# Kernel tuning notes

Measured on AMD Instinct MI355X. Metric: run time of the kernel, lower is better.

## Reference

```python
import jax, jax.numpy as jnp
import numpy as np

LOG_2PI = float(np.log(2.0 * np.pi))


def setup_inputs() -> dict:
    key = jax.random.key(0)
    k1, k2, k3 = jax.random.split(key, 3)
    N, M, D = 8192, 4096, 784
    samples = jax.random.normal(k1, (N, D), dtype=jnp.float32)
    x = jax.random.normal(k2, (M, D), dtype=jnp.float32)
    # per-feature std, kept away from zero for numerical sanity
    std = jax.random.uniform(k3, (D,), dtype=jnp.float32, minval=0.5, maxval=1.5)
    return {"samples": samples, "x": x, "std": std}


def reference(samples, x, std):
    # Diagonal-Gaussian mixture log-prob:
    #   logp[n, m] = sum_d [ -0.5*((s_nd - x_md)/std_d)^2 - 0.5*log(2*pi) - log(std_d) ]
    # computed via the ||u||^2 + ||v||^2 - 2 u.v identity on std-scaled vectors
    # (mathematically identical to the torch broadcast, without the (N,M,D) tensor).
    N, D = samples.shape
    M = x.shape[0]
    u = samples / std  # (N, D)
    v = x / std        # (M, D)
    sq_dist = (
        jnp.sum(u * u, axis=1)[:, None]
        + jnp.sum(v * v, axis=1)[None, :]
        - 2.0 * jnp.einsum("nd,md->nm", u, v)
    )  # (N, M)
    log_const = -0.5 * D * LOG_2PI - jnp.sum(jnp.log(std))
    log_prob = -0.5 * sq_dist + log_const  # (N, M)
    # logsumexp over mixture components, minus log(M)
    return jax.nn.logsumexp(log_prob, axis=1) - jnp.log(jnp.asarray(M, dtype=samples.dtype))
```

## Files before the change

### kernel.cpp

```cpp
#include <hip/hip_runtime.h>
#include <cstdint>
#include <cstddef>


#define N_ROWS 8192
#define M_ROWS 4096
#define D_DIM  784
#define KPB    896
#define LOG2PI 1.8378770664093453f
#define LOGM   8.317766166719343f

typedef unsigned char u8;
typedef __attribute__((ext_vector_type(8))) int   i32x8;
typedef __attribute__((ext_vector_type(4))) float f32x4;

__device__ __forceinline__ void gld16(const u8* g, u8* l) {
    __builtin_amdgcn_global_load_lds(
        (__attribute__((address_space(1))) void*)(void*)g,
        (__attribute__((address_space(3))) void*)l, 16, 0, 0);
}

__global__ __launch_bounds__(256) void k_prep(const float* __restrict__ samples,
                                              const float* __restrict__ x,
                                              const float* __restrict__ stdv,
                                              u8* __restrict__ dst,
                                              float* __restrict__ norm) {
    const int wid = threadIdx.x >> 6, lane = threadIdx.x & 63;
    const int row0 = blockIdx.x * 8 + wid * 2;

    float4 rstd[4];
#pragma unroll
    for (int i = 0; i < 4; ++i) {
        int c = lane + 64 * i;
        rstd[i] = make_float4(1.f, 1.f, 1.f, 1.f);
        if (c < 196) {
            float4 d = ((const float4*)stdv)[c];
            rstd[i] = make_float4(1.f / d.x, 1.f / d.y, 1.f / d.z, 1.f / d.w);
        }
    }

#pragma unroll
    for (int rr = 0; rr < 2; ++rr) {
        const int row = row0 + rr;
        const float* src = (row < N_ROWS) ? samples + (size_t)row * D_DIM
                                          : x + (size_t)(row - N_ROWS) * D_DIM;
        unsigned* drow = (unsigned*)(dst + (size_t)row * KPB);
        float sq = 0.f;
#pragma unroll
        for (int i = 0; i < 4; ++i) {
            const int c = lane + 64 * i;
            if (c < 224) {
                unsigned p = 0;
                if (c < 196) {
                    float4 s = ((const float4*)src)[c];
                    float ux = s.x * rstd[i].x, uy = s.y * rstd[i].y;
                    float uz = s.z * rstd[i].z, uw = s.w * rstd[i].w;
                    p = __builtin_amdgcn_cvt_pk_fp8_f32(ux, uy, 0, false);
                    p = __builtin_amdgcn_cvt_pk_fp8_f32(uz, uw, p, true);
                    float r0 = __builtin_amdgcn_cvt_f32_fp8(p, 0);
                    float r1 = __builtin_amdgcn_cvt_f32_fp8(p, 1);
                    float r2 = __builtin_amdgcn_cvt_f32_fp8(p, 2);
                    float r3 = __builtin_amdgcn_cvt_f32_fp8(p, 3);
                    sq += r0 * r0 + r1 * r1 + r2 * r2 + r3 * r3;
                }
                drow[c] = p;
            }
        }
        for (int m = 32; m; m >>= 1) sq += __shfl_xor(sq, m);
        if (lane == 0) norm[row] = sq;
    }
}

__global__ __launch_bounds__(512, 2) void k_gemm(const u8* __restrict__ U,
                                                 const u8* __restrict__ V,
                                                 const float* __restrict__ vnorm,
                                                 float* __restrict__ pmax,
                                                 float* __restrict__ psum) {
    __shared__ __align__(16) char smem[131072];
    float2* part = (float2*)smem;

    const int tid = threadIdx.x;
    const int lane = tid & 63;
    const int wid = tid >> 6;
    const int waveRow = wid >> 2;
    const int waveCol = wid & 3;
    const int bCol = blockIdx.x;
    const int bRow = blockIdx.y;
    const int g = lane >> 4, rl = lane & 15;

    const int r16 = lane >> 2, sl = lane & 3;
    const int gc16 = sl ^ ((r16 >> 1) & 3);
    const u8* gA[2]; const u8* gB[2]; int lo[2];
#pragma unroll
    for (int q = 0; q < 2; ++q) {
        const int rg = wid * 2 + q;
        gA[q] = U + (size_t)(bRow * 256 + rg * 16 + r16) * KPB + gc16 * 16;
        gB[q] = V + (size_t)(bCol * 256 + rg * 16 + r16) * KPB + gc16 * 16;
        lo[q] = rg * 1024;
    }

    const int key = (rl >> 1) & 3;
    const int slotLo = (2 * (g & 1)) ^ key;
    const int aoff = (g >> 1) * 32768 + (waveRow * 128 + rl) * 64 + slotLo * 16;
    const int boff = (g >> 1) * 32768 + 16384 + (waveCol * 64 + rl) * 64 + slotLo * 16;

    f32x4 acc[8][4];
#pragma unroll
    for (int i = 0; i < 8; ++i)
#pragma unroll
        for (int j = 0; j < 4; ++j) acc[i][j] = (f32x4){0.f, 0.f, 0.f, 0.f};

#define ISSUE(u) { \
    u8* lb = (u8*)smem + ((u) & 3) * 32768; \
    const int ko = (u) * 64; \
    gld16(gA[0] + ko, lb + lo[0]); \
    gld16(gB[0] + ko, lb + 16384 + lo[0]); \
    gld16(gA[1] + ko, lb + lo[1]); \
    gld16(gB[1] + ko, lb + 16384 + lo[1]); }

    ISSUE(0); ISSUE(1); ISSUE(2);

#pragma unroll
    for (int T = 0; T < 7; ++T) {
        if (T < 6) ISSUE(2 * T + 3);
        if (T < 6) __builtin_amdgcn_s_waitcnt(0x0F78);
        else       __builtin_amdgcn_s_waitcnt(0x0F70);
        __builtin_amdgcn_s_barrier();

        const char* base = smem + (T & 1) * 65536;
        i32x8 b[4], a[2];
#pragma unroll
        for (int ph = 0; ph < 4; ++ph) {
            if (ph == 0) {
#pragma unroll
                for (int j = 0; j < 4; ++j) {
                    int4 L = *(const int4*)(base + (boff + j * 1024));
                    int4 H = *(const int4*)(base + ((boff + j * 1024) ^ 16));
                    b[j] = (i32x8){L.x, L.y, L.z, L.w, H.x, H.y, H.z, H.w};
                }
            }
#pragma unroll
            for (int t = 0; t < 2; ++t) {
                const int i = ph * 2 + t;
                int4 L = *(const int4*)(base + (aoff + i * 1024));
                int4 H = *(const int4*)(base + ((aoff + i * 1024) ^ 16));
                a[t] = (i32x8){L.x, L.y, L.z, L.w, H.x, H.y, H.z, H.w};
            }
            __builtin_amdgcn_s_barrier();
            __builtin_amdgcn_s_waitcnt(0xC07F);
            __builtin_amdgcn_s_setprio(1);
#pragma unroll
            for (int t = 0; t < 2; ++t)
#pragma unroll
                for (int j = 0; j < 4; ++j)
                    acc[ph * 2 + t][j] = __builtin_amdgcn_mfma_scale_f32_16x16x128_f8f6f4(
                        a[t], b[j], acc[ph * 2 + t][j], 0 , 0 ,
                        0, 127 , 0, 127 );
            __builtin_amdgcn_s_setprio(0);
            __builtin_amdgcn_s_barrier();
        }
        if (T < 5) ISSUE(2 * T + 4);
    }
#undef ISSUE
    __syncthreads();

    float vn[4];
#pragma unroll
    for (int j = 0; j < 4; ++j) vn[j] = vnorm[bCol * 256 + waveCol * 64 + j * 16 + rl];

    const int prow0 = waveRow * 128 + g * 4;
    const int pc = waveCol * 16 + rl;
#pragma unroll
    for (int i = 0; i < 8; ++i) {
#pragma unroll
        for (int rg = 0; rg < 4; ++rg) {
            float w0 = acc[i][0][rg] - 0.5f * vn[0];
            float w1 = acc[i][1][rg] - 0.5f * vn[1];
            float w2 = acc[i][2][rg] - 0.5f * vn[2];
            float w3 = acc[i][3][rg] - 0.5f * vn[3];
            float m = fmaxf(fmaxf(w0, w1), fmaxf(w2, w3));
            float s = __expf(w0 - m) + __expf(w1 - m) + __expf(w2 - m) + __expf(w3 - m);
            part[(prow0 + i * 16 + rg) * 64 + pc] = make_float2(m, s);
        }
    }
    __syncthreads();
    if (tid < 256) {
        const float2* p = part + tid * 64;
        const int rot = tid & 63;
        float m = -3.4e38f;
#pragma unroll 8
        for (int q = 0; q < 64; ++q) m = fmaxf(m, p[(q + rot) & 63].x);
        float s = 0.f;
#pragma unroll 8
        for (int q = 0; q < 64; ++q) { float2 v = p[(q + rot) & 63]; s += v.y * __expf(v.x - m); }
        size_t grow = (size_t)(bRow * 256 + tid);
        pmax[grow * 16 + bCol] = m;
        psum[grow * 16 + bCol] = s;
    }
}

__global__ __launch_bounds__(256) void k_final(const float* __restrict__ pmax,
                                               const float* __restrict__ psum,
                                               const float* __restrict__ norm,
                                               const float* __restrict__ stdv,
                                               float* __restrict__ out) {
    __shared__ float wsum[4];
    const int t = threadIdx.x;
    float ls = 0.f;
    for (int d = t; d < D_DIM; d += 256) ls += logf(stdv[d]);
    for (int m = 32; m; m >>= 1) ls += __shfl_xor(ls, m);
    if ((t & 63) == 0) wsum[t >> 6] = ls;
    __syncthreads();
    const float logc = -0.5f * (float)D_DIM * LOG2PI - (wsum[0] + wsum[1] + wsum[2] + wsum[3]);

    const int n = blockIdx.x * 256 + t;
    const float* pm = pmax + (size_t)n * 16;
    const float* ps = psum + (size_t)n * 16;
    float gm = pm[0];
#pragma unroll
    for (int c = 1; c < 16; ++c) gm = fmaxf(gm, pm[c]);
    float S = 0.f;
#pragma unroll
    for (int c = 0; c < 16; ++c) S += ps[c] * __expf(pm[c] - gm);
    out[n] = gm + logf(S) - 0.5f * norm[n] + logc - LOGM;
}

extern "C" void kernel_launch(void* const* d_in, const int* in_sizes, int n_in,
                              void* d_out, int out_size, void* d_ws, size_t ws_size,
                              hipStream_t stream) {
    const float* samples = (const float*)d_in[0];
    const float* x       = (const float*)d_in[1];
    const float* stdv    = (const float*)d_in[2];
    float* out = (float*)d_out;

    char* ws = (char*)d_ws;
    u8*    U    = (u8*)ws;
    u8*    V    = (u8*)(ws + 7340032);
    float* norm = (float*)(ws + 11010048);
    float* pmax = (float*)(ws + 11059200);
    float* psum = (float*)(ws + 11583488);

    k_prep<<<(N_ROWS + M_ROWS) / 8, 256, 0, stream>>>(samples, x, stdv, U, norm);
    k_gemm<<<dim3(M_ROWS / 256, N_ROWS / 256), 512, 0, stream>>>(U, V, norm + N_ROWS, pmax, psum);
    k_final<<<N_ROWS / 256, 256, 0, stream>>>(pmax, psum, norm, stdv, out);
}
```

Measured before the change: 139.2 us.

## Switch GEMM to 32x32x64 FP8 MFMA with 3-stage LDS ring

```diff
diff --git a/kernel.cpp b/kernel.cpp
--- a/kernel.cpp
+++ b/kernel.cpp
@@ -11,8 +11,8 @@
 #define LOGM   8.317766166719343f
 
 typedef unsigned char u8;
-typedef __attribute__((ext_vector_type(8))) int   i32x8;
-typedef __attribute__((ext_vector_type(4))) float f32x4;
+typedef __attribute__((ext_vector_type(8)))  int   i32x8;
+typedef __attribute__((ext_vector_type(16))) float f32x16;
 
 __device__ __forceinline__ void gld16(const u8* g, u8* l) {
     __builtin_amdgcn_global_load_lds(
@@ -86,116 +86,122 @@
     const int waveCol = wid & 3;
     const int bCol = blockIdx.x;
     const int bRow = blockIdx.y;
-    const int g = lane >> 4, rl = lane & 15;
-
-    const int r16 = lane >> 2, sl = lane & 3;
-    const int gc16 = sl ^ ((r16 >> 1) & 3);
+    const int lr = lane & 31, h = lane >> 5;
+
+    const int r4 = lane >> 2;
+    const int gc = (lane & 3) ^ ((lane >> 3) & 3);
     const u8* gA[2]; const u8* gB[2]; int lo[2];
 #pragma unroll
     for (int q = 0; q < 2; ++q) {
-        const int rg = wid * 2 + q;
-        gA[q] = U + (size_t)(bRow * 256 + rg * 16 + r16) * KPB + gc16 * 16;
-        gB[q] = V + (size_t)(bCol * 256 + rg * 16 + r16) * KPB + gc16 * 16;
-        lo[q] = rg * 1024;
-    }
-
-    const int key = (rl >> 1) & 3;
-    const int slotLo = (2 * (g & 1)) ^ key;
-    const int aoff = (g >> 1) * 32768 + (waveRow * 128 + rl) * 64 + slotLo * 16;
-    const int boff = (g >> 1) * 32768 + 16384 + (waveCol * 64 + rl) * 64 + slotLo * 16;
-
-    f32x4 acc[8][4];
-#pragma unroll
-    for (int i = 0; i < 8; ++i)
-#pragma unroll
-        for (int j = 0; j < 4; ++j) acc[i][j] = (f32x4){0.f, 0.f, 0.f, 0.f};
+        const int row = wid * 32 + q * 16 + r4;
+        gA[q] = U + (size_t)(bRow * 256 + row) * KPB + gc * 16;
+        gB[q] = V + (size_t)(bCol * 256 + row) * KPB + gc * 16;
+        lo[q] = wid * 2048 + q * 1024;
+    }
+
+    const int key = (lr >> 1) & 3;
+    const int slotL = (2 * h) ^ key;
+    const int aoff = (waveRow * 128 + lr) * 64 + slotL * 16;
+    const int boff = 16384 + (waveCol * 64 + lr) * 64 + slotL * 16;
+
+    f32x16 acc[4][2];
+#pragma unroll
+    for (int i = 0; i < 4; ++i)
+#pragma unroll
+        for (int j = 0; j < 2; ++j)
+#pragma unroll
+            for (int r = 0; r < 16; ++r) acc[i][j][r] = 0.f;
 
 #define ISSUE(u) { \
-    u8* lb = (u8*)smem + ((u) & 3) * 32768; \
+    u8* lb = (u8*)smem + ((u) % 3) * 32768; \
     const int ko = (u) * 64; \
     gld16(gA[0] + ko, lb + lo[0]); \
     gld16(gB[0] + ko, lb + 16384 + lo[0]); \
     gld16(gA[1] + ko, lb + lo[1]); \
     gld16(gB[1] + ko, lb + 16384 + lo[1]); }
 
-    ISSUE(0); ISSUE(1); ISSUE(2);
-
-#pragma unroll
-    for (int T = 0; T < 7; ++T) {
-        if (T < 6) ISSUE(2 * T + 3);
-        if (T < 6) __builtin_amdgcn_s_waitcnt(0x0F78);
-        else       __builtin_amdgcn_s_waitcnt(0x0F70);
+    ISSUE(0); ISSUE(1);
+
+#pragma unroll
+    for (int kt = 0; kt < 14; ++kt) {
+        if (kt < 12) {
+            ISSUE(kt + 2);
+            __builtin_amdgcn_s_waitcnt(0x0F78);
+        } else if (kt == 12) {
+            __builtin_amdgcn_s_waitcnt(0x0F74);
+        } else {
+            __builtin_amdgcn_s_waitcnt(0x0F70);
+        }
         __builtin_amdgcn_s_barrier();
 
-        const char* base = smem + (T & 1) * 65536;
-        i32x8 b[4], a[2];
-#pragma unroll
-        for (int ph = 0; ph < 4; ++ph) {
-            if (ph == 0) {
-#pragma unroll
-                for (int j = 0; j < 4; ++j) {
-                    int4 L = *(const int4*)(base + (boff + j * 1024));
-                    int4 H = *(const int4*)(base + ((boff + j * 1024) ^ 16));
-                    b[j] = (i32x8){L.x, L.y, L.z, L.w, H.x, H.y, H.z, H.w};
-                }
+        const char* base = smem + (kt % 3) * 32768;
+        i32x8 a[4], b[2];
+#pragma unroll
+        for (int i = 0; i < 4; ++i) {
+            int4 L = *(const int4*)(base + (aoff + i * 2048));
+            int4 H = *(const int4*)(base + ((aoff + i * 2048) ^ 16));
+            a[i] = (i32x8){L.x, L.y, L.z, L.w, H.x, H.y, H.z, H.w};
+        }
+#pragma unroll
+        for (int j = 0; j < 2; ++j) {
+            int4 L = *(const int4*)(base + (boff + j * 2048));
+            int4 H = *(const int4*)(base + ((boff + j * 2048) ^ 16));
+            b[j] = (i32x8){L.x, L.y, L.z, L.w, H.x, H.y, H.z, H.w};
+        }
+#pragma unroll
+        for (int i = 0; i < 4; ++i)
+#pragma unroll
+            for (int j = 0; j < 2; ++j)
+                acc[i][j] = __builtin_amdgcn_mfma_scale_f32_32x32x64_f8f6f4(
+                    a[i], b[j], acc[i][j], 0 , 0 ,
+                    0, 127 , 0, 127 );
+
+        __builtin_amdgcn_s_barrier();
+    }
+#undef ISSUE
+
+    const float vn0 = vnorm[bCol * 256 + waveCol * 64 + lr];
+    const float vn1 = vnorm[bCol * 256 + waveCol * 64 + 32 + lr];
+    __syncthreads();
+
+#pragma unroll
+    for (int i = 0; i < 4; ++i) {
+#pragma unroll
+        for (int r = 0; r < 16; ++r) {
+            float w0 = acc[i][0][r] - 0.5f * vn0;
+            float w1 = acc[i][1][r] - 0.5f * vn1;
+            float m = fmaxf(w0, w1);
+            float s = __expf(w0 - m) + __expf(w1 - m);
+            float mo = __shfl_xor(m, 16);
+            float so = __shfl_xor(s, 16);
+            float M = fmaxf(m, mo);
+            s = s * __expf(m - M) + so * __expf(mo - M);
+            if (lr < 16) {
+                const int rin = (r & 3) + 8 * (r >> 2) + 4 * h;
+                part[(waveRow * 128 + i * 32 + rin) * 64 + (waveCol * 16 + lr)] =
+                    make_float2(M, s);
             }
-#pragma unroll
-            for (int t = 0; t < 2; ++t) {
-                const int i = ph * 2 + t;
-                int4 L = *(const int4*)(base + (aoff + i * 1024));
-                int4 H = *(const int4*)(base + ((aoff + i * 1024) ^ 16));
-                a[t] = (i32x8){L.x, L.y, L.z, L.w, H.x, H.y, H.z, H.w};
-            }
-            __builtin_amdgcn_s_barrier();
-            __builtin_amdgcn_s_waitcnt(0xC07F);
-            __builtin_amdgcn_s_setprio(1);
-#pragma unroll
-            for (int t = 0; t < 2; ++t)
-#pragma unroll
-                for (int j = 0; j < 4; ++j)
-                    acc[ph * 2 + t][j] = __builtin_amdgcn_mfma_scale_f32_16x16x128_f8f6f4(
-                        a[t], b[j], acc[ph * 2 + t][j], 0 , 0 ,
-                        0, 127 , 0, 127 );
-            __builtin_amdgcn_s_setprio(0);
-            __builtin_amdgcn_s_barrier();
-        }
-        if (T < 5) ISSUE(2 * T + 4);
-    }
-#undef ISSUE
+        }
+    }
     __syncthreads();
-
-    float vn[4];
-#pragma unroll
-    for (int j = 0; j < 4; ++j) vn[j] = vnorm[bCol * 256 + waveCol * 64 + j * 16 + rl];
-
-    const int prow0 = waveRow * 128 + g * 4;
-    const int pc = waveCol * 16 + rl;
-#pragma unroll
-    for (int i = 0; i < 8; ++i) {
-#pragma unroll
-        for (int rg = 0; rg < 4; ++rg) {
-            float w0 = acc[i][0][rg] - 0.5f * vn[0];
-            float w1 = acc[i][1][rg] - 0.5f * vn[1];
-            float w2 = acc[i][2][rg] - 0.5f * vn[2];
-            float w3 = acc[i][3][rg] - 0.5f * vn[3];
-            float m = fmaxf(fmaxf(w0, w1), fmaxf(w2, w3));
-            float s = __expf(w0 - m) + __expf(w1 - m) + __expf(w2 - m) + __expf(w3 - m);
-            part[(prow0 + i * 16 + rg) * 64 + pc] = make_float2(m, s);
-        }
-    }
-    __syncthreads();
-    if (tid < 256) {
-        const float2* p = part + tid * 64;
-        const int rot = tid & 63;
+    {
+        const int row = tid >> 1, half = tid & 1;
+        const float2* p = part + row * 64 + half * 32;
         float m = -3.4e38f;
 #pragma unroll 8
-        for (int q = 0; q < 64; ++q) m = fmaxf(m, p[(q + rot) & 63].x);
+        for (int q = 0; q < 32; ++q) m = fmaxf(m, p[(q + row) & 31].x);
         float s = 0.f;
 #pragma unroll 8
-        for (int q = 0; q < 64; ++q) { float2 v = p[(q + rot) & 63]; s += v.y * __expf(v.x - m); }
-        size_t grow = (size_t)(bRow * 256 + tid);
-        pmax[grow * 16 + bCol] = m;
-        psum[grow * 16 + bCol] = s;
+        for (int q = 0; q < 32; ++q) { float2 v = p[(q + row) & 31]; s += v.y * __expf(v.x - m); }
+        float mo = __shfl_xor(m, 1);
+        float so = __shfl_xor(s, 1);
+        float M = fmaxf(m, mo);
+        s = s * __expf(m - M) + so * __expf(mo - M);
+        if (half == 0) {
+            size_t grow = (size_t)(bRow * 256 + row);
+            pmax[grow * 16 + bCol] = M;
+            psum[grow * 16 + bCol] = s;
+        }
     }
 }
 
```

New measurement: 287.7 us. +106.7%, slower.

## Simplify GEMM main loop: whole-tile prefetch, single barrier, interleaved fragment loads

Applied to the files above, without the earlier changes.

```diff
diff --git a/kernel.cpp b/kernel.cpp
--- a/kernel.cpp
+++ b/kernel.cpp
@@ -88,21 +88,22 @@
     const int bRow = blockIdx.y;
     const int g = lane >> 4, rl = lane & 15;
 
-    const int r16 = lane >> 2, sl = lane & 3;
-    const int gc16 = sl ^ ((r16 >> 1) & 3);
-    const u8* gA[2]; const u8* gB[2]; int lo[2];
+    const int r4 = lane >> 2;
+    const int gc = (lane & 3) ^ ((lane >> 3) & 3);
+    const u8* gA[2]; int lo[2];
 #pragma unroll
     for (int q = 0; q < 2; ++q) {
-        const int rg = wid * 2 + q;
-        gA[q] = U + (size_t)(bRow * 256 + rg * 16 + r16) * KPB + gc16 * 16;
-        gB[q] = V + (size_t)(bCol * 256 + rg * 16 + r16) * KPB + gc16 * 16;
-        lo[q] = rg * 1024;
-    }
+        const int row = wid * 32 + q * 16 + r4;
+        gA[q] = U + (size_t)(bRow * 256 + row) * KPB + gc * 16;
+        lo[q] = wid * 2048 + q * 1024;
+    }
+    const ptrdiff_t dBA = (V - U) +
+        ((ptrdiff_t)bCol * 256 - (ptrdiff_t)bRow * 256) * (ptrdiff_t)KPB;
 
     const int key = (rl >> 1) & 3;
-    const int slotLo = (2 * (g & 1)) ^ key;
-    const int aoff = (g >> 1) * 32768 + (waveRow * 128 + rl) * 64 + slotLo * 16;
-    const int boff = (g >> 1) * 32768 + 16384 + (waveCol * 64 + rl) * 64 + slotLo * 16;
+    const int slotL = (2 * (g & 1)) ^ key;
+    const int aoff = (g >> 1) * 32768 + (waveRow * 128 + rl) * 64 + slotL * 16;
+    const int boff = (g >> 1) * 32768 + 16384 + (waveCol * 64 + rl) * 64 + slotL * 16;
 
     f32x4 acc[8][4];
 #pragma unroll
@@ -114,86 +115,84 @@
     u8* lb = (u8*)smem + ((u) & 3) * 32768; \
     const int ko = (u) * 64; \
     gld16(gA[0] + ko, lb + lo[0]); \
-    gld16(gB[0] + ko, lb + 16384 + lo[0]); \
+    gld16(gA[0] + dBA + ko, lb + 16384 + lo[0]); \
     gld16(gA[1] + ko, lb + lo[1]); \
-    gld16(gB[1] + ko, lb + 16384 + lo[1]); }
-
-    ISSUE(0); ISSUE(1); ISSUE(2);
+    gld16(gA[1] + dBA + ko, lb + 16384 + lo[1]); }
+
+#define ISSUE_TILE(T) { ISSUE(2*(T)); ISSUE(2*(T)+1); }
+
+#define LOADFRAG(dst, off) { \
+    int4 L_ = *(const int4*)(base + (off)); \
+    int4 H_ = *(const int4*)(base + ((off) ^ 16)); \
+    dst = (i32x8){L_.x, L_.y, L_.z, L_.w, H_.x, H_.y, H_.z, H_.w}; }
+
+    ISSUE_TILE(0); ISSUE_TILE(1);
 
 #pragma unroll
     for (int T = 0; T < 7; ++T) {
-        if (T < 6) ISSUE(2 * T + 3);
         if (T < 6) __builtin_amdgcn_s_waitcnt(0x0F78);
         else       __builtin_amdgcn_s_waitcnt(0x0F70);
         __builtin_amdgcn_s_barrier();
 
         const char* base = smem + (T & 1) * 65536;
-        i32x8 b[4], a[2];
-#pragma unroll
-        for (int ph = 0; ph < 4; ++ph) {
-            if (ph == 0) {
-#pragma unroll
-                for (int j = 0; j < 4; ++j) {
-                    int4 L = *(const int4*)(base + (boff + j * 1024));
-                    int4 H = *(const int4*)(base + ((boff + j * 1024) ^ 16));
-                    b[j] = (i32x8){L.x, L.y, L.z, L.w, H.x, H.y, H.z, H.w};
-                }
-            }
-#pragma unroll
-            for (int t = 0; t < 2; ++t) {
-                const int i = ph * 2 + t;
-                int4 L = *(const int4*)(base + (aoff + i * 1024));
-                int4 H = *(const int4*)(base + ((aoff + i * 1024) ^ 16));
-                a[t] = (i32x8){L.x, L.y, L.z, L.w, H.x, H.y, H.z, H.w};
-            }
-            __builtin_amdgcn_s_barrier();
-            __builtin_amdgcn_s_waitcnt(0xC07F);
-            __builtin_amdgcn_s_setprio(1);
-#pragma unroll
-            for (int t = 0; t < 2; ++t)
-#pragma unroll
-                for (int j = 0; j < 4; ++j)
-                    acc[ph * 2 + t][j] = __builtin_amdgcn_mfma_scale_f32_16x16x128_f8f6f4(
-                        a[t], b[j], acc[ph * 2 + t][j], 0 , 0 ,
-                        0, 127 , 0, 127 );
-            __builtin_amdgcn_s_setprio(0);
-            __builtin_amdgcn_s_barrier();
-        }
-        if (T < 5) ISSUE(2 * T + 4);
-    }
+        i32x8 b0, b1, b2, b3;
+        LOADFRAG(b0, boff);
+        LOADFRAG(b1, boff + 1024);
+        LOADFRAG(b2, boff + 2 * 1024);
+        LOADFRAG(b3, boff + 3 * 1024);
+#pragma unroll
+        for (int i = 0; i < 8; ++i) {
+            i32x8 ai;
+            LOADFRAG(ai, aoff + i * 1024);
+            acc[i][0] = __builtin_amdgcn_mfma_scale_f32_16x16x128_f8f6f4(
+                ai, b0, acc[i][0], 0, 0, 0, 127, 0, 127);
+            acc[i][1] = __builtin_amdgcn_mfma_scale_f32_16x16x128_f8f6f4(
+                ai, b1, acc[i][1], 0, 0, 0, 127, 0, 127);
+            acc[i][2] = __builtin_amdgcn_mfma_scale_f32_16x16x128_f8f6f4(
+                ai, b2, acc[i][2], 0, 0, 0, 127, 0, 127);
+            acc[i][3] = __builtin_amdgcn_mfma_scale_f32_16x16x128_f8f6f4(
+                ai, b3, acc[i][3], 0, 0, 0, 127, 0, 127);
+        }
+
+        __builtin_amdgcn_s_barrier();
+        if (T < 5) ISSUE_TILE(T + 2);
+    }
+#undef LOADFRAG
+#undef ISSUE_TILE
 #undef ISSUE
+
+    float vn[4];
+#pragma unroll
+    for (int j = 0; j < 4; ++j) vn[j] = vnorm[bCol * 256 + waveCol * 64 + j * 16 + rl];
     __syncthreads();
-
-    float vn[4];
-#pragma unroll
-    for (int j = 0; j < 4; ++j) vn[j] = vnorm[bCol * 256 + waveCol * 64 + j * 16 + rl];
 
     const int prow0 = waveRow * 128 + g * 4;
     const int pc = waveCol * 16 + rl;
 #pragma unroll
     for (int i = 0; i < 8; ++i) {
 #pragma unroll
-        for (int rg = 0; rg < 4; ++rg) {
-            float w0 = acc[i][0][rg] - 0.5f * vn[0];
-            float w1 = acc[i][1][rg] - 0.5f * vn[1];
-            float w2 = acc[i][2][rg] - 0.5f * vn[2];
-            float w3 = acc[i][3][rg] - 0.5f * vn[3];
+        for (int r = 0; r < 4; ++r) {
+            float w0 = acc[i][0][r] - 0.5f * vn[0];
+            float w1 = acc[i][1][r] - 0.5f * vn[1];
+            float w2 = acc[i][2][r] - 0.5f * vn[2];
+            float w3 = acc[i][3][r] - 0.5f * vn[3];
             float m = fmaxf(fmaxf(w0, w1), fmaxf(w2, w3));
             float s = __expf(w0 - m) + __expf(w1 - m) + __expf(w2 - m) + __expf(w3 - m);
-            part[(prow0 + i * 16 + rg) * 64 + pc] = make_float2(m, s);
+            part[(prow0 + i * 16 + r) * 64 + pc] = make_float2(m, s);
         }
     }
     __syncthreads();
     if (tid < 256) {
-        const float2* p = part + tid * 64;
-        const int rot = tid & 63;
+        const int row = tid;
+        const float2* p = part + row * 64;
+        const int rot = row & 63;
         float m = -3.4e38f;
 #pragma unroll 8
         for (int q = 0; q < 64; ++q) m = fmaxf(m, p[(q + rot) & 63].x);
         float s = 0.f;
 #pragma unroll 8
         for (int q = 0; q < 64; ++q) { float2 v = p[(q + rot) & 63]; s += v.y * __expf(v.x - m); }
-        size_t grow = (size_t)(bRow * 256 + tid);
+        size_t grow = (size_t)(bRow * 256 + row);
         pmax[grow * 16 + bCol] = m;
         psum[grow * 16 + bCol] = s;
     }
```

After: 135.9 us. -2.3%, faster.
